# Kernel optimization log

Hardware: AMD Instinct MI355X
Metric: run time of the kernel (lower is better)

## Reference

```python
import jax, jax.numpy as jnp
import numpy as np

N_NODES = 100000
N_EDGES = 1600000
D = 64


def setup_inputs() -> dict:
    key = jax.random.key(0)
    ks = jax.random.split(key, 6)
    x = jax.random.normal(ks[0], (N_NODES, D), dtype=jnp.float32)
    edge_index = jax.random.randint(ks[1], (2, N_EDGES), 0, N_NODES, dtype=jnp.int64)
    W1 = jax.random.normal(ks[2], (D, D), dtype=jnp.float32) / np.sqrt(D)
    b1 = jax.random.normal(ks[3], (D,), dtype=jnp.float32) * 0.02
    W2 = jax.random.normal(ks[4], (D, D), dtype=jnp.float32) / np.sqrt(D)
    b2 = jax.random.normal(ks[5], (D,), dtype=jnp.float32) * 0.02
    return {"x": x, "edge_index": edge_index, "W1": W1, "b1": b1, "W2": W2, "b2": b2}


def _gcn_conv(x, W, b, src, dst, norm, n_nodes):
    # PyG GCNConv: h = X W; out_i = sum_{j->i} norm_ji * h_j; out += b
    h = x @ W                                   # [N, D]
    msgs = h[src] * norm[:, None]               # [E+N, D] gather
    out = jax.ops.segment_sum(msgs, dst, num_segments=n_nodes)  # scatter-add
    return out + b


def reference(x, edge_index, W1, b1, W2, b2):
    n = x.shape[0]
    # add self-loops (GCNConv default add_self_loops=True)
    loop = jnp.arange(n, dtype=edge_index.dtype)
    src = jnp.concatenate([edge_index[0], loop])
    dst = jnp.concatenate([edge_index[1], loop])
    # symmetric normalization D^{-1/2} (A+I) D^{-1/2}
    deg = jax.ops.segment_sum(jnp.ones_like(src, dtype=x.dtype), dst, num_segments=n)
    dinv = jax.lax.rsqrt(deg)                   # deg >= 1 due to self-loops
    norm = dinv[src] * dinv[dst]                # [E+N]
    h = _gcn_conv(x, W1, b1, src, dst, norm, n)
    h = jax.nn.relu(h)
    out = _gcn_conv(h, W2, b2, src, dst, norm, n)
    return out
```

## Files before the change

kernel.cpp:

```cpp
#include <hip/hip_runtime.h>

#define FDIM   64
#define BSHIFT 9
#define BNODES 512
#define BCAP   8960
#define EPB    4096
#define LPAD   72

typedef unsigned short bf16_t;
typedef __attribute__((ext_vector_type(8))) short bf16x8;
typedef __attribute__((ext_vector_type(4))) float f32x4;
typedef __attribute__((ext_vector_type(2))) float f32x2;

__device__ __forceinline__ unsigned f2bf(float f) {
    unsigned u = __float_as_uint(f);
    u += 0x7FFFu + ((u >> 16) & 1u);
    return u >> 16;
}
__device__ __forceinline__ float bflo(unsigned u) { return __uint_as_float(u << 16); }
__device__ __forceinline__ float bfhi(unsigned u) { return __uint_as_float(u & 0xFFFF0000u); }

__device__ __forceinline__ f32x2 bfpair(unsigned u) {
    f32x2 r;
    r.x = __uint_as_float(u << 16);
    r.y = __uint_as_float(u);
    return r;
}
__device__ __forceinline__ void addbf8p(f32x2* acc, uint4 v) {
    acc[0] += bfpair(v.x);
    acc[1] += bfpair(v.y);
    acc[2] += bfpair(v.z);
    acc[3] += bfpair(v.w);
}

__global__ void k_zero(int* __restrict__ g) { g[threadIdx.x] = 0; }

__global__ __launch_bounds__(256) void k_bucket(const int* __restrict__ src,
                                                const int* __restrict__ dst,
                                                int* __restrict__ gCursor,
                                                unsigned* __restrict__ pairs,
                                                int E, int N) {
    __shared__ int cnt4[4][256];
    __shared__ int cur4[4][256];
    const int t  = threadIdx.x;
    const int w  = t >> 6;
    const int e0 = blockIdx.x * EPB;
    int dcache[EPB / 256];
    #pragma unroll
    for (int i = 0; i < 4; ++i) cnt4[i][t] = 0;
    __syncthreads();

    #pragma unroll 4
    for (int i = 0; i < EPB / 256; ++i) {
        int e = e0 + i * 256 + t;
        int d = -1;
        if (e < E) {
            d = dst[e];
            d = min(max(d, 0), N - 1);
            atomicAdd(&cnt4[w][d >> BSHIFT], 1);
        }
        dcache[i] = d;
    }
    __syncthreads();
    {
        int c0 = cnt4[0][t], c1 = cnt4[1][t], c2 = cnt4[2][t], c3 = cnt4[3][t];
        int tot = c0 + c1 + c2 + c3;
        int b = 0;
        if (tot > 0) b = atomicAdd(&gCursor[t], tot);
        cur4[0][t] = b;
        cur4[1][t] = b + c0;
        cur4[2][t] = b + c0 + c1;
        cur4[3][t] = b + c0 + c1 + c2;
    }
    __syncthreads();
    #pragma unroll 4
    for (int i = 0; i < EPB / 256; ++i) {
        int d = dcache[i];
        if (d >= 0) {
            int e = e0 + i * 256 + t;
            int s = src[e];
            s = min(max(s, 0), N - 1);
            int bk = d >> BSHIFT;
            int slot = atomicAdd(&cur4[w][bk], 1);
            if (slot < BCAP)
                pairs[(size_t)bk * BCAP + slot] =
                    ((unsigned)(d & (BNODES - 1)) << 17) | (unsigned)s;
        }
    }
}

__global__ __launch_bounds__(1024) void k_sort(unsigned* __restrict__ pairs,
                                               const int* __restrict__ gCursor,
                                               float* __restrict__ dinv,
                                               int* __restrict__ beg,
                                               int* __restrict__ endp,
                                               int N) {
    __shared__ unsigned buf[BCAP];
    __shared__ int cnt4[4][BNODES];
    __shared__ int scn[BNODES];
    __shared__ int cur4[4][BNODES];
    const int b = blockIdx.x, t = threadIdx.x;
    const int grp = t >> 8;
    const int count = min(gCursor[b], BCAP);
    unsigned* p = pairs + (size_t)b * BCAP;

    ((int*)cnt4)[t] = 0;
    ((int*)cnt4)[t + 1024] = 0;
    __syncthreads();
    for (int i = t; i < count; i += 1024) {
        unsigned pk = p[i];
        buf[i] = pk;
        atomicAdd(&cnt4[grp][pk >> 17], 1);
    }
    __syncthreads();
    if (t < BNODES) scn[t] = cnt4[0][t] + cnt4[1][t] + cnt4[2][t] + cnt4[3][t];
    __syncthreads();
    for (int off = 1; off < BNODES; off <<= 1) {
        int v = 0;
        if (t < BNODES && t >= off) v = scn[t - off];
        __syncthreads();
        if (t < BNODES) scn[t] += v;
        __syncthreads();
    }
    if (t < BNODES) {
        int c0 = cnt4[0][t], c1 = cnt4[1][t], c2 = cnt4[2][t], c3 = cnt4[3][t];
        int tot = c0 + c1 + c2 + c3;
        int st  = scn[t] - tot;
        cur4[0][t] = st;
        cur4[1][t] = st + c0;
        cur4[2][t] = st + c0 + c1;
        cur4[3][t] = st + c0 + c1 + c2;
        int n = (b << BSHIFT) + t;
        if (n < N) {
            beg[n]  = b * BCAP + st;
            endp[n] = b * BCAP + st + tot;
            dinv[n] = rsqrtf((float)(tot + 1));
        }
    }
    __syncthreads();
    for (int i = t; i < count; i += 1024) {
        unsigned pk = buf[i];
        int pos = atomicAdd(&cur4[grp][pk >> 17], 1);
        p[pos] = pk & 0x1FFFFu;
    }
}

__device__ __forceinline__ void mfma_core(const bf16_t* Xs, const bf16_t* Wt,
                                          const float* __restrict__ dinv,
                                          bf16_t* __restrict__ Ob,
                                          int base, int N, int tid) {
    const int l  = tid & 63;
    const int w  = tid >> 6;
    const int lm = l & 15;
    const int lk = l >> 4;

    f32x4 acc[4];
    #pragma unroll
    for (int ct = 0; ct < 4; ++ct) acc[ct] = (f32x4){0.f, 0.f, 0.f, 0.f};

    #pragma unroll
    for (int kc = 0; kc < 2; ++kc) {
        bf16x8 a = *reinterpret_cast<const bf16x8*>(&Xs[(16 * w + lm) * LPAD + 32 * kc + 8 * lk]);
        #pragma unroll
        for (int ct = 0; ct < 4; ++ct) {
            bf16x8 b = *reinterpret_cast<const bf16x8*>(&Wt[(16 * ct + lm) * LPAD + 32 * kc + 8 * lk]);
            acc[ct] = __builtin_amdgcn_mfma_f32_16x16x32_bf16(a, b, acc[ct], 0, 0, 0);
        }
    }

    float dv[4];
    #pragma unroll
    for (int j = 0; j < 4; ++j) {
        int gr = base + 16 * w + 4 * lk + j;
        dv[j] = (gr < N) ? dinv[gr] : 0.f;
    }
    #pragma unroll
    for (int ct = 0; ct < 4; ++ct) {
        #pragma unroll
        for (int j = 0; j < 4; ++j) {
            int gr = base + 16 * w + 4 * lk + j;
            if (gr < N)
                Ob[(size_t)gr * FDIM + 16 * ct + lm] = (bf16_t)f2bf(acc[ct][j] * dv[j]);
        }
    }
}

__device__ __forceinline__ void stage_w_t(const float* __restrict__ W, bf16_t* Wt, int tid) {
    #pragma unroll
    for (int i = 0; i < 4; ++i) {
        int idx = tid + i * 256;
        int k  = idx >> 4;
        int c4 = (idx & 15) * 4;
        float4 v = reinterpret_cast<const float4*>(W)[idx];
        Wt[(c4 + 0) * LPAD + k] = (bf16_t)f2bf(v.x);
        Wt[(c4 + 1) * LPAD + k] = (bf16_t)f2bf(v.y);
        Wt[(c4 + 2) * LPAD + k] = (bf16_t)f2bf(v.z);
        Wt[(c4 + 3) * LPAD + k] = (bf16_t)f2bf(v.w);
    }
}

__global__ __launch_bounds__(256) void k_gemm_f32(const float* __restrict__ X,
                                                  const float* __restrict__ W,
                                                  const float* __restrict__ dinv,
                                                  bf16_t* __restrict__ Ob, int N) {
    __shared__ bf16_t Xs[64 * LPAD];
    __shared__ bf16_t Wt[64 * LPAD];
    const int tid  = threadIdx.x;
    const int base = blockIdx.x * 64;

    stage_w_t(W, Wt, tid);
    #pragma unroll
    for (int i = 0; i < 2; ++i) {
        int idx = tid + i * 256;
        int r = idx >> 3, c8 = (idx & 7) * 8;
        int gr = base + r;
        float4 v0 = make_float4(0.f, 0.f, 0.f, 0.f), v1 = v0;
        if (gr < N) {
            v0 = reinterpret_cast<const float4*>(X)[(size_t)gr * 16 + (idx & 7) * 2];
            v1 = reinterpret_cast<const float4*>(X)[(size_t)gr * 16 + (idx & 7) * 2 + 1];
        }
        uint4 o;
        o.x = f2bf(v0.x) | (f2bf(v0.y) << 16);
        o.y = f2bf(v0.z) | (f2bf(v0.w) << 16);
        o.z = f2bf(v1.x) | (f2bf(v1.y) << 16);
        o.w = f2bf(v1.z) | (f2bf(v1.w) << 16);
        *reinterpret_cast<uint4*>(&Xs[r * LPAD + c8]) = o;
    }
    __syncthreads();
    mfma_core(Xs, Wt, dinv, Ob, base, N, tid);
}

__global__ __launch_bounds__(256) void k_gemm_bf16(const bf16_t* __restrict__ Y,
                                                   const float* __restrict__ W,
                                                   const float* __restrict__ dinv,
                                                   bf16_t* __restrict__ Ob, int N) {
    __shared__ bf16_t Xs[64 * LPAD];
    __shared__ bf16_t Wt[64 * LPAD];
    const int tid  = threadIdx.x;
    const int base = blockIdx.x * 64;

    stage_w_t(W, Wt, tid);
    #pragma unroll
    for (int i = 0; i < 2; ++i) {
        int idx = tid + i * 256;
        int r = idx >> 3, c8 = (idx & 7) * 8;
        int gr = base + r;
        uint4 v = make_uint4(0u, 0u, 0u, 0u);
        if (gr < N) v = reinterpret_cast<const uint4*>(Y)[(size_t)gr * 8 + (idx & 7)];
        *reinterpret_cast<uint4*>(&Xs[r * LPAD + c8]) = v;
    }
    __syncthreads();
    mfma_core(Xs, Wt, dinv, Ob, base, N, tid);
}

__global__ __launch_bounds__(256) void k_agg(const bf16_t* __restrict__ Hs,
                                             const int* __restrict__ srcList,
                                             const int* __restrict__ beg,
                                             const int* __restrict__ endp,
                                             const float* __restrict__ dinv,
                                             const float* __restrict__ bias,
                                             float* __restrict__ Of,
                                             bf16_t* __restrict__ Ob,
                                             int N, int do_relu) {
    const int lane = threadIdx.x & 63;
    const int w    = threadIdx.x >> 6;
    const int g    = lane >> 3;
    const int c8   = lane & 7;
    const int node = (blockIdx.x * 4 + w) * 8 + g;

    const uint4* Hv = reinterpret_cast<const uint4*>(Hs) + c8;

    int kb = 0, ke = 0;
    if (node < N) { kb = beg[node]; ke = endp[node]; }

    f32x2 acc[4];
    #pragma unroll
    for (int i = 0; i < 4; ++i) acc[i] = (f32x2){0.f, 0.f};

    int k = kb;
    for (; k + 7 < ke; k += 8) {
        int s0 = srcList[k],     s1 = srcList[k + 1];
        int s2 = srcList[k + 2], s3 = srcList[k + 3];
        int s4 = srcList[k + 4], s5 = srcList[k + 5];
        int s6 = srcList[k + 6], s7 = srcList[k + 7];
        uint4 h0 = Hv[(size_t)s0 * 8];
        uint4 h1 = Hv[(size_t)s1 * 8];
        uint4 h2 = Hv[(size_t)s2 * 8];
        uint4 h3 = Hv[(size_t)s3 * 8];
        uint4 h4 = Hv[(size_t)s4 * 8];
        uint4 h5 = Hv[(size_t)s5 * 8];
        uint4 h6 = Hv[(size_t)s6 * 8];
        uint4 h7 = Hv[(size_t)s7 * 8];
        addbf8p(acc, h0); addbf8p(acc, h1); addbf8p(acc, h2); addbf8p(acc, h3);
        addbf8p(acc, h4); addbf8p(acc, h5); addbf8p(acc, h6); addbf8p(acc, h7);
    }
    if (k + 3 < ke) {
        int s0 = srcList[k],     s1 = srcList[k + 1];
        int s2 = srcList[k + 2], s3 = srcList[k + 3];
        uint4 h0 = Hv[(size_t)s0 * 8];
        uint4 h1 = Hv[(size_t)s1 * 8];
        uint4 h2 = Hv[(size_t)s2 * 8];
        uint4 h3 = Hv[(size_t)s3 * 8];
        addbf8p(acc, h0); addbf8p(acc, h1); addbf8p(acc, h2); addbf8p(acc, h3);
        k += 4;
    }
    for (; k < ke; ++k) {
        uint4 h0 = Hv[(size_t)srcList[k] * 8];
        addbf8p(acc, h0);
    }

    if (node >= N) return;

    uint4 sv = Hv[(size_t)node * 8];
    acc[0].x += bflo(sv.x); acc[0].y += bfhi(sv.x);
    acc[1].x += bflo(sv.y); acc[1].y += bfhi(sv.y);
    acc[2].x += bflo(sv.z); acc[2].y += bfhi(sv.z);
    acc[3].x += bflo(sv.w); acc[3].y += bfhi(sv.w);

    const float di = dinv[node];
    const float4* bv = reinterpret_cast<const float4*>(bias);
    float4 b0 = bv[c8 * 2], b1 = bv[c8 * 2 + 1];
    float r[8];
    r[0] = fmaf(di, acc[0].x, b0.x); r[1] = fmaf(di, acc[0].y, b0.y);
    r[2] = fmaf(di, acc[1].x, b0.z); r[3] = fmaf(di, acc[1].y, b0.w);
    r[4] = fmaf(di, acc[2].x, b1.x); r[5] = fmaf(di, acc[2].y, b1.y);
    r[6] = fmaf(di, acc[3].x, b1.z); r[7] = fmaf(di, acc[3].y, b1.w);
    if (do_relu) {
        #pragma unroll
        for (int i = 0; i < 8; ++i) r[i] = fmaxf(r[i], 0.f);
    }
    if (Ob) {
        uint4 o;
        o.x = f2bf(r[0]) | (f2bf(r[1]) << 16);
        o.y = f2bf(r[2]) | (f2bf(r[3]) << 16);
        o.z = f2bf(r[4]) | (f2bf(r[5]) << 16);
        o.w = f2bf(r[6]) | (f2bf(r[7]) << 16);
        reinterpret_cast<uint4*>(Ob)[(size_t)node * 8 + c8] = o;
    } else {
        float4 o0 = make_float4(r[0], r[1], r[2], r[3]);
        float4 o1 = make_float4(r[4], r[5], r[6], r[7]);
        reinterpret_cast<float4*>(Of)[(size_t)node * 16 + c8 * 2]     = o0;
        reinterpret_cast<float4*>(Of)[(size_t)node * 16 + c8 * 2 + 1] = o1;
    }
}

extern "C" void kernel_launch(void* const* d_in, const int* in_sizes, int n_in,
                              void* d_out, int out_size, void* d_ws, size_t ws_size,
                              hipStream_t stream) {
    const float* x  = (const float*)d_in[0];
    const int*   ei = (const int*)  d_in[1];
    const float* W1 = (const float*)d_in[2];
    const float* b1 = (const float*)d_in[3];
    const float* W2 = (const float*)d_in[4];
    const float* b2 = (const float*)d_in[5];
    float* out = (float*)d_out;

    const int N = in_sizes[0] / FDIM;
    const int E = in_sizes[1] / 2;
    const int* src = ei;
    const int* dst = ei + E;

    const int nB = (N + BNODES - 1) >> BSHIFT;

    auto align1k = [](size_t v) { return (v + 1023) & ~(size_t)1023; };
    char* p = (char*)d_ws;
    int*      gCursor = (int*)p;        p += align1k(256 * 4);
    float*    dinv    = (float*)p;      p += align1k((size_t)N * 4);
    int*      beg     = (int*)p;        p += align1k((size_t)N * 4);
    int*      endp    = (int*)p;        p += align1k((size_t)N * 4);
    unsigned* pairs   = (unsigned*)p;   p += align1k((size_t)nB * BCAP * 4);
    bf16_t*   H       = (bf16_t*)p;     p += align1k((size_t)N * FDIM * 2);
    bf16_t*   Y       = (bf16_t*)p;

    k_zero<<<1, 256, 0, stream>>>(gCursor);
    k_bucket<<<(E + EPB - 1) / EPB, 256, 0, stream>>>(src, dst, gCursor, pairs, E, N);
    k_sort<<<nB, 1024, 0, stream>>>(pairs, gCursor, dinv, beg, endp, N);

    const int gemmBlocks = (N + 63) / 64;
    const int aggBlocks  = (N + 31) / 32;
    const int* srcList = (const int*)pairs;

    k_gemm_f32<<<gemmBlocks, 256, 0, stream>>>(x, W1, dinv, H, N);
    k_agg<<<aggBlocks, 256, 0, stream>>>(H, srcList, beg, endp, dinv, b1,
                                         nullptr, Y, N, 1);

    k_gemm_bf16<<<gemmBlocks, 256, 0, stream>>>(Y, W2, dinv, H, N);
    k_agg<<<aggBlocks, 256, 0, stream>>>(H, srcList, beg, endp, dinv, b2,
                                         out, nullptr, N, 0);
}
```

Baseline: 137.0 us.

## Fuse layer-1 aggregation with layer-2 GEMM into one kernel

```diff
diff --git a/kernel.cpp b/kernel.cpp
--- a/kernel.cpp
+++ b/kernel.cpp
@@ -230,24 +230,94 @@
     mfma_core(Xs, Wt, dinv, Ob, base, N, tid);
 }
 
-__global__ __launch_bounds__(256) void k_gemm_bf16(const bf16_t* __restrict__ Y,
-                                                   const float* __restrict__ W,
-                                                   const float* __restrict__ dinv,
-                                                   bf16_t* __restrict__ Ob, int N) {
+__global__ __launch_bounds__(256) void k_aggemm(const bf16_t* __restrict__ Hs,
+                                                const int* __restrict__ srcList,
+                                                const int* __restrict__ beg,
+                                                const int* __restrict__ endp,
+                                                const float* __restrict__ dinv,
+                                                const float* __restrict__ bias,
+                                                const float* __restrict__ W2,
+                                                bf16_t* __restrict__ Ob, int N) {
     __shared__ bf16_t Xs[64 * LPAD];
     __shared__ bf16_t Wt[64 * LPAD];
     const int tid  = threadIdx.x;
     const int base = blockIdx.x * 64;
 
-    stage_w_t(W, Wt, tid);
-    #pragma unroll
-    for (int i = 0; i < 2; ++i) {
-        int idx = tid + i * 256;
-        int r = idx >> 3, c8 = (idx & 7) * 8;
-        int gr = base + r;
-        uint4 v = make_uint4(0u, 0u, 0u, 0u);
-        if (gr < N) v = reinterpret_cast<const uint4*>(Y)[(size_t)gr * 8 + (idx & 7)];
-        *reinterpret_cast<uint4*>(&Xs[r * LPAD + c8]) = v;
+    stage_w_t(W2, Wt, tid);
+
+    const int lane = tid & 63;
+    const int w    = tid >> 6;
+    const int g    = lane >> 3;
+    const int c8   = lane & 7;
+    const uint4* Hv = reinterpret_cast<const uint4*>(Hs) + c8;
+    const float4* bv = reinterpret_cast<const float4*>(bias);
+    const float4 b0 = bv[c8 * 2], b1v = bv[c8 * 2 + 1];
+
+    #pragma unroll
+    for (int half = 0; half < 2; ++half) {
+        const int rowL = w * 16 + half * 8 + g;
+        const int node = base + rowL;
+        int kb = 0, ke = 0;
+        if (node < N) { kb = beg[node]; ke = endp[node]; }
+
+        f32x2 acc[4];
+        #pragma unroll
+        for (int i = 0; i < 4; ++i) acc[i] = (f32x2){0.f, 0.f};
+
+        int k = kb;
+        for (; k + 7 < ke; k += 8) {
+            int s0 = srcList[k],     s1 = srcList[k + 1];
+            int s2 = srcList[k + 2], s3 = srcList[k + 3];
+            int s4 = srcList[k + 4], s5 = srcList[k + 5];
+            int s6 = srcList[k + 6], s7 = srcList[k + 7];
+            uint4 h0 = Hv[(size_t)s0 * 8];
+            uint4 h1 = Hv[(size_t)s1 * 8];
+            uint4 h2 = Hv[(size_t)s2 * 8];
+            uint4 h3 = Hv[(size_t)s3 * 8];
+            uint4 h4 = Hv[(size_t)s4 * 8];
+            uint4 h5 = Hv[(size_t)s5 * 8];
+            uint4 h6 = Hv[(size_t)s6 * 8];
+            uint4 h7 = Hv[(size_t)s7 * 8];
+            addbf8p(acc, h0); addbf8p(acc, h1); addbf8p(acc, h2); addbf8p(acc, h3);
+            addbf8p(acc, h4); addbf8p(acc, h5); addbf8p(acc, h6); addbf8p(acc, h7);
+        }
+        if (k + 3 < ke) {
+            int s0 = srcList[k],     s1 = srcList[k + 1];
+            int s2 = srcList[k + 2], s3 = srcList[k + 3];
+            uint4 h0 = Hv[(size_t)s0 * 8];
+            uint4 h1 = Hv[(size_t)s1 * 8];
+            uint4 h2 = Hv[(size_t)s2 * 8];
+            uint4 h3 = Hv[(size_t)s3 * 8];
+            addbf8p(acc, h0); addbf8p(acc, h1); addbf8p(acc, h2); addbf8p(acc, h3);
+            k += 4;
+        }
+        for (; k < ke; ++k) {
+            uint4 h0 = Hv[(size_t)srcList[k] * 8];
+            addbf8p(acc, h0);
+        }
+
+        uint4 o = make_uint4(0u, 0u, 0u, 0u);
+        if (node < N) {
+            uint4 sv = Hv[(size_t)node * 8];
+            acc[0].x += bflo(sv.x); acc[0].y += bfhi(sv.x);
+            acc[1].x += bflo(sv.y); acc[1].y += bfhi(sv.y);
+            acc[2].x += bflo(sv.z); acc[2].y += bfhi(sv.z);
+            acc[3].x += bflo(sv.w); acc[3].y += bfhi(sv.w);
+            const float di = dinv[node];
+            float r0 = fmaxf(fmaf(di, acc[0].x, b0.x), 0.f);
+            float r1 = fmaxf(fmaf(di, acc[0].y, b0.y), 0.f);
+            float r2 = fmaxf(fmaf(di, acc[1].x, b0.z), 0.f);
+            float r3 = fmaxf(fmaf(di, acc[1].y, b0.w), 0.f);
+            float r4 = fmaxf(fmaf(di, acc[2].x, b1v.x), 0.f);
+            float r5 = fmaxf(fmaf(di, acc[2].y, b1v.y), 0.f);
+            float r6 = fmaxf(fmaf(di, acc[3].x, b1v.z), 0.f);
+            float r7 = fmaxf(fmaf(di, acc[3].y, b1v.w), 0.f);
+            o.x = f2bf(r0) | (f2bf(r1) << 16);
+            o.y = f2bf(r2) | (f2bf(r3) << 16);
+            o.z = f2bf(r4) | (f2bf(r5) << 16);
+            o.w = f2bf(r6) | (f2bf(r7) << 16);
+        }
+        *reinterpret_cast<uint4*>(&Xs[rowL * LPAD + c8 * 8]) = o;
     }
     __syncthreads();
     mfma_core(Xs, Wt, dinv, Ob, base, N, tid);
@@ -260,8 +330,7 @@
                                              const float* __restrict__ dinv,
                                              const float* __restrict__ bias,
                                              float* __restrict__ Of,
-                                             bf16_t* __restrict__ Ob,
-                                             int N, int do_relu) {
+                                             int N) {
     const int lane = threadIdx.x & 63;
     const int w    = threadIdx.x >> 6;
     const int g    = lane >> 3;
@@ -320,28 +389,13 @@
     const float di = dinv[node];
     const float4* bv = reinterpret_cast<const float4*>(bias);
     float4 b0 = bv[c8 * 2], b1 = bv[c8 * 2 + 1];
-    float r[8];
-    r[0] = fmaf(di, acc[0].x, b0.x); r[1] = fmaf(di, acc[0].y, b0.y);
-    r[2] = fmaf(di, acc[1].x, b0.z); r[3] = fmaf(di, acc[1].y, b0.w);
-    r[4] = fmaf(di, acc[2].x, b1.x); r[5] = fmaf(di, acc[2].y, b1.y);
-    r[6] = fmaf(di, acc[3].x, b1.z); r[7] = fmaf(di, acc[3].y, b1.w);
-    if (do_relu) {
-        #pragma unroll
-        for (int i = 0; i < 8; ++i) r[i] = fmaxf(r[i], 0.f);
-    }
-    if (Ob) {
-        uint4 o;
-        o.x = f2bf(r[0]) | (f2bf(r[1]) << 16);
-        o.y = f2bf(r[2]) | (f2bf(r[3]) << 16);
-        o.z = f2bf(r[4]) | (f2bf(r[5]) << 16);
-        o.w = f2bf(r[6]) | (f2bf(r[7]) << 16);
-        reinterpret_cast<uint4*>(Ob)[(size_t)node * 8 + c8] = o;
-    } else {
-        float4 o0 = make_float4(r[0], r[1], r[2], r[3]);
-        float4 o1 = make_float4(r[4], r[5], r[6], r[7]);
-        reinterpret_cast<float4*>(Of)[(size_t)node * 16 + c8 * 2]     = o0;
-        reinterpret_cast<float4*>(Of)[(size_t)node * 16 + c8 * 2 + 1] = o1;
-    }
+    float4 o0, o1;
+    o0.x = fmaf(di, acc[0].x, b0.x); o0.y = fmaf(di, acc[0].y, b0.y);
+    o0.z = fmaf(di, acc[1].x, b0.z); o0.w = fmaf(di, acc[1].y, b0.w);
+    o1.x = fmaf(di, acc[2].x, b1.x); o1.y = fmaf(di, acc[2].y, b1.y);
+    o1.z = fmaf(di, acc[3].x, b1.z); o1.w = fmaf(di, acc[3].y, b1.w);
+    reinterpret_cast<float4*>(Of)[(size_t)node * 16 + c8 * 2]     = o0;
+    reinterpret_cast<float4*>(Of)[(size_t)node * 16 + c8 * 2 + 1] = o1;
 }
 
 extern "C" void kernel_launch(void* const* d_in, const int* in_sizes, int n_in,
@@ -370,7 +424,7 @@
     int*      endp    = (int*)p;        p += align1k((size_t)N * 4);
     unsigned* pairs   = (unsigned*)p;   p += align1k((size_t)nB * BCAP * 4);
     bf16_t*   H       = (bf16_t*)p;     p += align1k((size_t)N * FDIM * 2);
-    bf16_t*   Y       = (bf16_t*)p;
+    bf16_t*   H2      = (bf16_t*)p;
 
     k_zero<<<1, 256, 0, stream>>>(gCursor);
     k_bucket<<<(E + EPB - 1) / EPB, 256, 0, stream>>>(src, dst, gCursor, pairs, E, N);
@@ -381,10 +435,6 @@
     const int* srcList = (const int*)pairs;
 
     k_gemm_f32<<<gemmBlocks, 256, 0, stream>>>(x, W1, dinv, H, N);
-    k_agg<<<aggBlocks, 256, 0, stream>>>(H, srcList, beg, endp, dinv, b1,
-                                         nullptr, Y, N, 1);
-
-    k_gemm_bf16<<<gemmBlocks, 256, 0, stream>>>(Y, W2, dinv, H, N);
-    k_agg<<<aggBlocks, 256, 0, stream>>>(H, srcList, beg, endp, dinv, b2,
-                                         out, nullptr, N, 0);
-}
+    k_aggemm<<<gemmBlocks, 256, 0, stream>>>(H, srcList, beg, endp, dinv, b1, W2, H2, N);
+    k_agg<<<aggBlocks, 256, 0, stream>>>(H2, srcList, beg, endp, dinv, b2, out, N);
+}
```

Result: no change. 139.0 us (+1.4%).
